# Kernel optimization log

Hardware: AMD Instinct MI355X
Metric: run time of the kernel (lower is better)

## Reference

```python
import jax, jax.numpy as jnp
import numpy as np

B, T, D, E, K = 4, 4096, 4096, 64, 2
EPS = 1e-9

def setup_inputs() -> dict:
    key = jax.random.key(0)
    kx, kw = jax.random.split(key)
    x = jax.random.normal(kx, (B, T, D), dtype=jnp.float32)
    # router weight, init std=0.01 as in the torch module
    W = jax.random.normal(kw, (E, D), dtype=jnp.float32) * 0.01
    return {"x": x, "W": W}

def reference(x, W):
    b, t, d = x.shape
    x_flat = x.reshape(b * t, d)                      # (BT, D)
    logits = jnp.einsum('nd,ed->ne', x_flat, W)       # (BT, E)
    router_probs = jax.nn.softmax(logits, axis=-1)    # (BT, E)
    top_k_weights_raw, top_k_indices = jax.lax.top_k(router_probs, K)  # (BT, K)
    top_k_weights = top_k_weights_raw / (jnp.sum(top_k_weights_raw, axis=-1, keepdims=True) + EPS)
    return router_probs, top_k_indices, top_k_weights
```

## Files before the change

kernel.cpp:

```cpp
#include <hip/hip_runtime.h>

#define BT 16384
#define DK 4096
#define NE 64
#define BM 32
#define NSTG 32
#define NPROBS (BT * NE)
#define NIDX (NPROBS)
#define NWTS (NPROBS + BT * 2)

typedef __bf16 bf16x8 __attribute__((ext_vector_type(8)));
typedef float f32x16 __attribute__((ext_vector_type(16)));

__device__ __forceinline__ unsigned asu(float f) { return __builtin_bit_cast(unsigned, f); }
__device__ __forceinline__ float asf(unsigned u) { return __builtin_bit_cast(float, u); }

__device__ __forceinline__ void gl_lds16(const void* g, void* l) {
    __builtin_amdgcn_global_load_lds(
        (const __attribute__((address_space(1))) unsigned int*)g,
        (__attribute__((address_space(3))) unsigned int*)l, 16, 0, 0);
}

__device__ __forceinline__ void split3(const float* xx, uint4* pl) {
    unsigned h0[8], h1[8], h2[8];
#pragma unroll
    for (int j = 0; j < 8; ++j) {
        const float xf = xx[j];
        const unsigned a0 = asu(xf) & 0xFFFF0000u;
        const float r1 = xf - asf(a0);
        const unsigned a1 = asu(r1) & 0xFFFF0000u;
        const float r2 = r1 - asf(a1);
        const unsigned a2 = asu(r2) & 0xFFFF0000u;
        h0[j] = a0; h1[j] = a1; h2[j] = a2;
    }
    pl[0] = make_uint4((h0[0] >> 16) | (h0[1] & 0xFFFF0000u), (h0[2] >> 16) | (h0[3] & 0xFFFF0000u),
                       (h0[4] >> 16) | (h0[5] & 0xFFFF0000u), (h0[6] >> 16) | (h0[7] & 0xFFFF0000u));
    pl[1] = make_uint4((h1[0] >> 16) | (h1[1] & 0xFFFF0000u), (h1[2] >> 16) | (h1[3] & 0xFFFF0000u),
                       (h1[4] >> 16) | (h1[5] & 0xFFFF0000u), (h1[6] >> 16) | (h1[7] & 0xFFFF0000u));
    pl[2] = make_uint4((h2[0] >> 16) | (h2[1] & 0xFFFF0000u), (h2[2] >> 16) | (h2[3] & 0xFFFF0000u),
                       (h2[4] >> 16) | (h2[5] & 0xFFFF0000u), (h2[6] >> 16) | (h2[7] & 0xFFFF0000u));
}

__global__ __launch_bounds__(256) void w_prep(
    const float* __restrict__ W, uint4* __restrict__ WF)
{
    const int g  = blockIdx.x * 256 + threadIdx.x;
    const int e  = g >> 9;
    const int kg = g & 511;
    const float4 v0 = *(const float4*)(W + (long)e * DK + kg * 8);
    const float4 v1 = *(const float4*)(W + (long)e * DK + kg * 8 + 4);
    float xx[8] = {v0.x, v0.y, v0.z, v0.w, v1.x, v1.y, v1.z, v1.w};
    uint4 pl[3];
    split3(xx, pl);
    const int kst = kg >> 1;
    const int l   = (e & 31) | ((kg & 1) << 5);
    const int eh  = e >> 5;
#pragma unroll
    for (int p = 0; p < 3; ++p)
        WF[(long)kst * 384 + eh * 192 + p * 64 + l] = pl[p];
}

__global__ __launch_bounds__(512) void token_router(
    const float* __restrict__ x, const uint4* __restrict__ WF,
    float* __restrict__ out)
{
    __shared__ float4 xs4[2 * 4 * 256];
    __shared__ float  lg[BM * 68 + 2 * BM];

    const int tid  = threadIdx.x;
    const int wv   = tid >> 6;
    const int lane = tid & 63;
    const int eh   = wv & 1;
    const int kh   = wv >> 1;
    const long rowbase = (long)blockIdx.x * BM;

    const int sr = lane >> 3, sq = lane & 7;
    const float* gxa = x + (rowbase + (wv & 3) * 8 + sr) * (long)DK
                         + (wv >> 2) * 1024 + ((sq ^ sr) << 2);
    const float* gxb = gxa + 2048;
    const int dsta = (wv >> 2) * 256 + (wv & 3) * 64 + lane;
    const int dstb = dsta + 512;

    const int rr  = lane & 31;
    const int rsw = rr & 7;
    const int xbase = kh * 256 + rr * 8;

    const uint4* wfl = WF + eh * 192 + lane;

    f32x16 acc;
#pragma unroll
    for (int i = 0; i < 16; ++i) acc[i] = 0.f;

    uint4 bc0, bc1, bc2, bn0, bn1, bn2;

    gl_lds16(gxa, xs4 + dsta);
    gl_lds16(gxb, xs4 + dstb);
    {
        const long k0 = (long)(kh * 64) * 384;
        bc0 = wfl[k0]; bc1 = wfl[k0 + 64]; bc2 = wfl[k0 + 128];
    }
    __syncthreads();

#define COMPUTE(PB, T, B0r, B1r, B2r) do {                                    \
    const int qb = (T) * 4 + (lane >> 5) * 2;                                 \
    const float4 alo = xs4[(PB) + xbase + (qb ^ rsw)];                        \
    const float4 ahi = xs4[(PB) + xbase + ((qb + 1) ^ rsw)];                  \
    float xx[8] = {alo.x, alo.y, alo.z, alo.w, ahi.x, ahi.y, ahi.z, ahi.w};   \
    uint4 pl[3];                                                              \
    split3(xx, pl);                                                           \
    const bf16x8 A0 = __builtin_bit_cast(bf16x8, pl[0]);                      \
    const bf16x8 A1 = __builtin_bit_cast(bf16x8, pl[1]);                      \
    const bf16x8 A2 = __builtin_bit_cast(bf16x8, pl[2]);                      \
    const bf16x8 B0 = __builtin_bit_cast(bf16x8, B0r);                        \
    const bf16x8 B1 = __builtin_bit_cast(bf16x8, B1r);                        \
    const bf16x8 B2 = __builtin_bit_cast(bf16x8, B2r);                        \
    acc = __builtin_amdgcn_mfma_f32_32x32x16_bf16(A0, B0, acc, 0, 0, 0);      \
    acc = __builtin_amdgcn_mfma_f32_32x32x16_bf16(A0, B1, acc, 0, 0, 0);      \
    acc = __builtin_amdgcn_mfma_f32_32x32x16_bf16(A1, B0, acc, 0, 0, 0);      \
    acc = __builtin_amdgcn_mfma_f32_32x32x16_bf16(A1, B1, acc, 0, 0, 0);      \
    acc = __builtin_amdgcn_mfma_f32_32x32x16_bf16(A0, B2, acc, 0, 0, 0);      \
    acc = __builtin_amdgcn_mfma_f32_32x32x16_bf16(A2, B0, acc, 0, 0, 0);      \
} while (0)

    for (int s = 0; s < NSTG; ++s) {
        const int pb = (s & 1) * 1024;
        const int nb = pb ^ 1024;
        if (s + 1 < NSTG) {
            gl_lds16(gxa + (s + 1) * 32, xs4 + nb + dsta);
            gl_lds16(gxb + (s + 1) * 32, xs4 + nb + dstb);
        }
        {
            const long kn = ((long)(kh * 64 + s * 2 + 1)) * 384;
            bn0 = wfl[kn]; bn1 = wfl[kn + 64]; bn2 = wfl[kn + 128];
            COMPUTE(pb, 0, bc0, bc1, bc2);
        }
        {
            if (s + 1 < NSTG) {
                const long kn = ((long)(kh * 64 + (s + 1) * 2)) * 384;
                bc0 = wfl[kn]; bc1 = wfl[kn + 64]; bc2 = wfl[kn + 128];
            }
            COMPUTE(pb, 1, bn0, bn1, bn2);
        }
        __syncthreads();
    }
#undef COMPUTE

#pragma unroll
    for (int ph = 0; ph < 4; ++ph) {
        if (kh == ph) {
            const int col = eh * 32 + (lane & 31);
            const int rbase = 4 * (lane >> 5);
#pragma unroll
            for (int rg = 0; rg < 16; ++rg) {
                const int row = (rg & 3) + 8 * (rg >> 2) + rbase;
                if (ph == 0) lg[row * 68 + col]  = acc[rg];
                else         lg[row * 68 + col] += acc[rg];
            }
        }
        __syncthreads();
    }

    float* rowm   = lg + BM * 68;
    float* rowinv = rowm + BM;
    if (tid < BM) {
        const int row = tid;
        float m = -3.4e38f;
        for (int e = 0; e < NE; ++e) m = fmaxf(m, lg[row * 68 + e]);
        float s = 0.f;
        float v1 = -1.f, v2 = -1.f;
        int   i1 = 0,    i2 = 0;
        for (int e = 0; e < NE; ++e) {
            const float p = __expf(lg[row * 68 + e] - m);
            s += p;
            if (p > v1)      { v2 = v1; i2 = i1; v1 = p; i1 = e; }
            else if (p > v2) { v2 = p; i2 = e; }
        }
        const float inv = 1.f / s;
        rowm[row]   = m;
        rowinv[row] = inv;
        const long grow = rowbase + row;
        const float p1 = v1 * inv, p2 = v2 * inv;
        const float dn = p1 + p2 + 1e-9f;
        out[NIDX + grow * 2 + 0] = (float)i1;
        out[NIDX + grow * 2 + 1] = (float)i2;
        out[NWTS + grow * 2 + 0] = p1 / dn;
        out[NWTS + grow * 2 + 1] = p2 / dn;
    }
    __syncthreads();

    {
        const int row = tid >> 4;
        const int e0  = (tid & 15) << 2;
        const float m = rowm[row], inv = rowinv[row];
        const long grow = rowbase + row;
        const float4 l4 = *reinterpret_cast<const float4*>(&lg[row * 68 + e0]);
        float4 p;
        p.x = __expf(l4.x - m) * inv;
        p.y = __expf(l4.y - m) * inv;
        p.z = __expf(l4.z - m) * inv;
        p.w = __expf(l4.w - m) * inv;
        *reinterpret_cast<float4*>(&out[grow * (long)NE + e0]) = p;
    }
}

extern "C" void kernel_launch(void* const* d_in, const int* in_sizes, int n_in,
                              void* d_out, int out_size, void* d_ws, size_t ws_size,
                              hipStream_t stream) {
    const float* x = (const float*)d_in[0];
    const float* W = (const float*)d_in[1];
    float* out = (float*)d_out;
    uint4* WF  = (uint4*)d_ws;

    w_prep<<<dim3(128), dim3(256), 0, stream>>>(W, WF);
    token_router<<<dim3(BT / BM), dim3(512), 0, stream>>>(x, WF, out);
}
```

Before: 90.54 us.

## Double rows per block to 64 and split K across 8 waves

Each block now handles 64 token rows with 1024 threads. Every wave keeps two 32x32 accumulators, so each loaded W fragment and its split is reused for two row tiles, halving W traffic per token. The x staging buffer in LDS grows to 128KB and is reused as the logits buffer afterwards. In exchange the grid has half as many blocks (256), the cross-wave K reduction takes 8 phases, and register pressure rises.

```diff
diff --git a/kernel.cpp b/kernel.cpp
--- a/kernel.cpp
+++ b/kernel.cpp
@@ -3,8 +3,8 @@
 #define BT 16384
 #define DK 4096
 #define NE 64
-#define BM 32
-#define NSTG 32
+#define BM 64
+#define NSTG 16
 #define NPROBS (BT * NE)
 #define NIDX (NPROBS)
 #define NWTS (NPROBS + BT * 2)
@@ -60,12 +60,12 @@
         WF[(long)kst * 384 + eh * 192 + p * 64 + l] = pl[p];
 }
 
-__global__ __launch_bounds__(512) void token_router(
+__global__ __launch_bounds__(1024) void token_router(
     const float* __restrict__ x, const uint4* __restrict__ WF,
     float* __restrict__ out)
 {
-    __shared__ float4 xs4[2 * 4 * 256];
-    __shared__ float  lg[BM * 68 + 2 * BM];
+    __shared__ float4 xs4[2 * 4096];
+    __shared__ float  rowm[BM], rowinv[BM];
 
     const int tid  = threadIdx.x;
     const int wv   = tid >> 6;
@@ -75,93 +75,119 @@
     const long rowbase = (long)blockIdx.x * BM;
 
     const int sr = lane >> 3, sq = lane & 7;
-    const float* gxa = x + (rowbase + (wv & 3) * 8 + sr) * (long)DK
-                         + (wv >> 2) * 1024 + ((sq ^ sr) << 2);
-    const float* gxb = gxa + 2048;
-    const int dsta = (wv >> 2) * 256 + (wv & 3) * 64 + lane;
-    const int dstb = dsta + 512;
-
-    const int rr  = lane & 31;
-    const int rsw = rr & 7;
-    const int xbase = kh * 256 + rr * 8;
+    const float* gx[4];
+    int dst[4];
+#pragma unroll
+    for (int i = 0; i < 4; ++i) {
+        const int u  = wv * 4 + i;
+        const int sl = u >> 3;
+        const int rg = u & 7;
+        gx[i]  = x + (rowbase + rg * 8 + sr) * (long)DK + sl * 512 + ((sq ^ sr) << 2);
+        dst[i] = sl * 512 + rg * 64 + lane;
+    }
+
+    const int rlo  = lane & 31;
+    const int rsw  = rlo & 7;
+    const int baseL = kh * 512 + rlo * 8;
+    const int baseH = baseL + 256;
 
     const uint4* wfl = WF + eh * 192 + lane;
 
-    f32x16 acc;
-#pragma unroll
-    for (int i = 0; i < 16; ++i) acc[i] = 0.f;
+    f32x16 accL, accH;
+#pragma unroll
+    for (int i = 0; i < 16; ++i) { accL[i] = 0.f; accH[i] = 0.f; }
 
     uint4 bc0, bc1, bc2, bn0, bn1, bn2;
 
-    gl_lds16(gxa, xs4 + dsta);
-    gl_lds16(gxb, xs4 + dstb);
+#pragma unroll
+    for (int i = 0; i < 4; ++i)
+        gl_lds16(gx[i], xs4 + dst[i]);
     {
-        const long k0 = (long)(kh * 64) * 384;
+        const long k0 = (long)(kh * 32) * 384;
         bc0 = wfl[k0]; bc1 = wfl[k0 + 64]; bc2 = wfl[k0 + 128];
     }
     __syncthreads();
 
-#define COMPUTE(PB, T, B0r, B1r, B2r) do {                                    \
+#define COMPUTE2(PB, T, B0r, B1r, B2r) do {                                   \
     const int qb = (T) * 4 + (lane >> 5) * 2;                                 \
-    const float4 alo = xs4[(PB) + xbase + (qb ^ rsw)];                        \
-    const float4 ahi = xs4[(PB) + xbase + ((qb + 1) ^ rsw)];                  \
-    float xx[8] = {alo.x, alo.y, alo.z, alo.w, ahi.x, ahi.y, ahi.z, ahi.w};   \
-    uint4 pl[3];                                                              \
-    split3(xx, pl);                                                           \
-    const bf16x8 A0 = __builtin_bit_cast(bf16x8, pl[0]);                      \
-    const bf16x8 A1 = __builtin_bit_cast(bf16x8, pl[1]);                      \
-    const bf16x8 A2 = __builtin_bit_cast(bf16x8, pl[2]);                      \
+    const float4 aloL = xs4[(PB) + baseL + (qb ^ rsw)];                       \
+    const float4 ahiL = xs4[(PB) + baseL + ((qb + 1) ^ rsw)];                 \
+    const float4 aloH = xs4[(PB) + baseH + (qb ^ rsw)];                       \
+    const float4 ahiH = xs4[(PB) + baseH + ((qb + 1) ^ rsw)];                 \
+    float xxL[8] = {aloL.x, aloL.y, aloL.z, aloL.w, ahiL.x, ahiL.y, ahiL.z, ahiL.w}; \
+    float xxH[8] = {aloH.x, aloH.y, aloH.z, aloH.w, ahiH.x, ahiH.y, ahiH.z, ahiH.w}; \
+    uint4 plL[3], plH[3];                                                     \
+    split3(xxL, plL);                                                         \
+    split3(xxH, plH);                                                         \
+    const bf16x8 AL0 = __builtin_bit_cast(bf16x8, plL[0]);                    \
+    const bf16x8 AL1 = __builtin_bit_cast(bf16x8, plL[1]);                    \
+    const bf16x8 AL2 = __builtin_bit_cast(bf16x8, plL[2]);                    \
+    const bf16x8 AH0 = __builtin_bit_cast(bf16x8, plH[0]);                    \
+    const bf16x8 AH1 = __builtin_bit_cast(bf16x8, plH[1]);                    \
+    const bf16x8 AH2 = __builtin_bit_cast(bf16x8, plH[2]);                    \
     const bf16x8 B0 = __builtin_bit_cast(bf16x8, B0r);                        \
     const bf16x8 B1 = __builtin_bit_cast(bf16x8, B1r);                        \
     const bf16x8 B2 = __builtin_bit_cast(bf16x8, B2r);                        \
-    acc = __builtin_amdgcn_mfma_f32_32x32x16_bf16(A0, B0, acc, 0, 0, 0);      \
-    acc = __builtin_amdgcn_mfma_f32_32x32x16_bf16(A0, B1, acc, 0, 0, 0);      \
-    acc = __builtin_amdgcn_mfma_f32_32x32x16_bf16(A1, B0, acc, 0, 0, 0);      \
-    acc = __builtin_amdgcn_mfma_f32_32x32x16_bf16(A1, B1, acc, 0, 0, 0);      \
-    acc = __builtin_amdgcn_mfma_f32_32x32x16_bf16(A0, B2, acc, 0, 0, 0);      \
-    acc = __builtin_amdgcn_mfma_f32_32x32x16_bf16(A2, B0, acc, 0, 0, 0);      \
+    accL = __builtin_amdgcn_mfma_f32_32x32x16_bf16(AL0, B0, accL, 0, 0, 0);   \
+    accL = __builtin_amdgcn_mfma_f32_32x32x16_bf16(AL0, B1, accL, 0, 0, 0);   \
+    accL = __builtin_amdgcn_mfma_f32_32x32x16_bf16(AL1, B0, accL, 0, 0, 0);   \
+    accL = __builtin_amdgcn_mfma_f32_32x32x16_bf16(AL1, B1, accL, 0, 0, 0);   \
+    accL = __builtin_amdgcn_mfma_f32_32x32x16_bf16(AL0, B2, accL, 0, 0, 0);   \
+    accL = __builtin_amdgcn_mfma_f32_32x32x16_bf16(AL2, B0, accL, 0, 0, 0);   \
+    accH = __builtin_amdgcn_mfma_f32_32x32x16_bf16(AH0, B0, accH, 0, 0, 0);   \
+    accH = __builtin_amdgcn_mfma_f32_32x32x16_bf16(AH0, B1, accH, 0, 0, 0);   \
+    accH = __builtin_amdgcn_mfma_f32_32x32x16_bf16(AH1, B0, accH, 0, 0, 0);   \
+    accH = __builtin_amdgcn_mfma_f32_32x32x16_bf16(AH1, B1, accH, 0, 0, 0);   \
+    accH = __builtin_amdgcn_mfma_f32_32x32x16_bf16(AH0, B2, accH, 0, 0, 0);   \
+    accH = __builtin_amdgcn_mfma_f32_32x32x16_bf16(AH2, B0, accH, 0, 0, 0);   \
 } while (0)
 
     for (int s = 0; s < NSTG; ++s) {
-        const int pb = (s & 1) * 1024;
-        const int nb = pb ^ 1024;
+        const int pb = (s & 1) * 4096;
+        const int nb = pb ^ 4096;
         if (s + 1 < NSTG) {
-            gl_lds16(gxa + (s + 1) * 32, xs4 + nb + dsta);
-            gl_lds16(gxb + (s + 1) * 32, xs4 + nb + dstb);
+#pragma unroll
+            for (int i = 0; i < 4; ++i)
+                gl_lds16(gx[i] + (s + 1) * 32, xs4 + nb + dst[i]);
         }
         {
-            const long kn = ((long)(kh * 64 + s * 2 + 1)) * 384;
+            const long kn = ((long)(kh * 32 + s * 2 + 1)) * 384;
             bn0 = wfl[kn]; bn1 = wfl[kn + 64]; bn2 = wfl[kn + 128];
-            COMPUTE(pb, 0, bc0, bc1, bc2);
+            COMPUTE2(pb, 0, bc0, bc1, bc2);
         }
         {
             if (s + 1 < NSTG) {
-                const long kn = ((long)(kh * 64 + (s + 1) * 2)) * 384;
+                const long kn = ((long)(kh * 32 + (s + 1) * 2)) * 384;
                 bc0 = wfl[kn]; bc1 = wfl[kn + 64]; bc2 = wfl[kn + 128];
             }
-            COMPUTE(pb, 1, bn0, bn1, bn2);
+            COMPUTE2(pb, 1, bn0, bn1, bn2);
         }
         __syncthreads();
     }
-#undef COMPUTE
-
-#pragma unroll
-    for (int ph = 0; ph < 4; ++ph) {
+#undef COMPUTE2
+
+    float* lg = (float*)xs4;
+
+#pragma unroll
+    for (int ph = 0; ph < 8; ++ph) {
         if (kh == ph) {
             const int col = eh * 32 + (lane & 31);
             const int rbase = 4 * (lane >> 5);
 #pragma unroll
             for (int rg = 0; rg < 16; ++rg) {
                 const int row = (rg & 3) + 8 * (rg >> 2) + rbase;
-                if (ph == 0) lg[row * 68 + col]  = acc[rg];
-                else         lg[row * 68 + col] += acc[rg];
+                if (ph == 0) {
+                    lg[row * 68 + col]        = accL[rg];
+                    lg[(row + 32) * 68 + col] = accH[rg];
+                } else {
+                    lg[row * 68 + col]        += accL[rg];
+                    lg[(row + 32) * 68 + col] += accH[rg];
+                }
             }
         }
         __syncthreads();
     }
 
-    float* rowm   = lg + BM * 68;
-    float* rowinv = rowm + BM;
     if (tid < BM) {
         const int row = tid;
         float m = -3.4e38f;
@@ -212,5 +238,5 @@
     uint4* WF  = (uint4*)d_ws;
 
     w_prep<<<dim3(128), dim3(256), 0, stream>>>(W, WF);
-    token_router<<<dim3(BT / BM), dim3(512), 0, stream>>>(x, WF, out);
-}
+    token_router<<<dim3(BT / BM), dim3(1024), 0, stream>>>(x, WF, out);
+}
```

Result: faster. 86.99 us (-3.9%).
